# Performance work log

Measured on AMD Instinct MI355X. Metric: run time of the kernel, lower is better.

## Reference

```python
import jax, jax.numpy as jnp
import numpy as np

ALPHA = 0.2  # LeakyReLU negative slope
EPS = 1e-8


def setup_inputs() -> dict:
    key = jax.random.key(0)
    ks = jax.random.split(key, 7)
    N, Fin, Fout, E = 100000, 256, 128, 800000
    node_embedding = jax.random.normal(ks[0], (N, Fin), dtype=jnp.float32)
    adj_pos = jax.random.randint(ks[1], (2, E), 0, N, dtype=jnp.int64)
    adj_neg = jax.random.randint(ks[2], (2, E), 0, N, dtype=jnp.int64)
    edge_embedding = jax.random.normal(ks[3], (2, Fout), dtype=jnp.float32)
    Wr = jax.random.normal(ks[4], (2, Fin, Fout), dtype=jnp.float32) * 0.05
    a = jax.random.normal(ks[5], (1, 2 * Fout), dtype=jnp.float32) * 0.05
    bias = jax.random.normal(ks[6], (1, Fout), dtype=jnp.float32) * 0.05
    return dict(node_embedding=node_embedding, edge_embedding=edge_embedding,
                Wr=Wr, a=a, bias=bias, adj_pos=adj_pos, adj_neg=adj_neg)


def reference(node_embedding, edge_embedding, Wr, a, bias, adj_pos, adj_neg):
    N = node_embedding.shape[0]
    Fout = Wr.shape[2]
    # h_r = X @ Wr[r], then column-scale by edge_embedding[r] (== mm with diag)
    h_pos = (node_embedding @ Wr[0]) * edge_embedding[0]  # [N, Fout]
    h_neg = (node_embedding @ Wr[1]) * edge_embedding[1]  # [N, Fout]
    a_src = a[0, :Fout]  # attention weights for source half of concat
    a_dst = a[0, Fout:]  # attention weights for dest half

    def edge_scores(h, adj):
        # a . [h[src], h[dst]] computed as node-level dots then scalar gather
        s = h @ a_src  # [N]
        d = h @ a_dst  # [N]
        z = s[adj[0]] + d[adj[1]]  # [E]
        z = jnp.where(z > 0, z, ALPHA * z)  # LeakyReLU
        return jax.nn.sigmoid(z)

    e_pos = edge_scores(h_pos, adj_pos)  # [E_pos]
    e_neg = edge_scores(h_neg, adj_neg)  # [E_neg]

    # row-sum normalizer: spmm(edge, edge_e, ones) == segment_sum over row idx
    rows = jnp.concatenate([adj_pos[0], adj_neg[0]])
    e_all = jnp.concatenate([e_pos, e_neg])
    row_sum = jax.ops.segment_sum(e_all, rows, num_segments=N) + EPS  # [N]

    # weighted aggregation: out[i] = sum_{(i,j)} e_ij * h[j]
    agg = (jax.ops.segment_sum(e_pos[:, None] * h_pos[adj_pos[1]], adj_pos[0], num_segments=N)
           + jax.ops.segment_sum(e_neg[:, None] * h_neg[adj_neg[1]], adj_neg[0], num_segments=N))
    return agg / row_sum[:, None] + bias
```

## Files before the change

### kernel.cpp

```cpp
#include <hip/hip_runtime.h>

#define ALPHA 0.2f
#define EPSV 1e-8f
#define BUCK_BITS 8
#define BUCK (1 << BUCK_BITS)
#define CAP 5120
#define EPB_A 4096
#define EPT_A (EPB_A / 256)

typedef float f32x4 __attribute__((ext_vector_type(4)));
typedef short bf16x8 __attribute__((ext_vector_type(8)));

static __device__ __forceinline__ unsigned short f2bf(float f) {
    union { float f; unsigned int u; } c; c.f = f;
    unsigned int u = c.u;
    unsigned int round = ((u >> 16) & 1) + 0x7FFF;
    return (unsigned short)((u + round) >> 16);
}
static __device__ __forceinline__ float bflo(unsigned int u) {
    union { unsigned int u; float f; } c; c.u = u << 16; return c.f;
}
static __device__ __forceinline__ float bfhi(unsigned int u) {
    union { unsigned int u; float f; } c; c.u = u & 0xFFFF0000u; return c.f;
}

__global__ __launch_bounds__(256) void convB_binA_kernel(
    const float* __restrict__ Wr, uint4* __restrict__ Bp,
    const int* __restrict__ adj_pos, const int* __restrict__ adj_neg,
    int* __restrict__ bucketCount, unsigned int* __restrict__ edges_tmp,
    int N, int E)
{
    __shared__ int hist[512];
    __shared__ int base[512];
    __shared__ int cur[512];
    const int tid = threadIdx.x;

    if ((int)blockIdx.x < 32) {
        const int t = blockIdx.x * 256 + tid;
        const int kb  = t >> 8;
        const int col = t & 255;
        const int rel = col >> 7;
        const int cc  = col & 127;
        unsigned short v[8];
        #pragma unroll
        for (int jj = 0; jj < 8; ++jj) {
            const int k = kb * 8 + jj;
            v[jj] = f2bf(Wr[(size_t)rel * 256 * 128 + (size_t)k * 128 + cc]);
        }
        Bp[t] = *reinterpret_cast<const uint4*>(v);
        return;
    }

    const int bb = blockIdx.x - 32;
    const long long e0 = (long long)bb * EPB_A;
    const long long twoE = 2LL * E;

    hist[tid] = 0;
    hist[tid + 256] = 0;

    int esrc[EPT_A];
    unsigned int erec[EPT_A];
    #pragma unroll
    for (int k = 0; k < EPT_A; ++k) {
        const long long idx = e0 + (long long)k * 256 + tid;
        if (idx < twoE) {
            const int rel = (idx >= E) ? 1 : 0;
            const long long eidx = rel ? idx - E : idx;
            const int* __restrict__ adj = rel ? adj_neg : adj_pos;
            const int src = adj[eidx];
            const int dst = adj[E + eidx];
            esrc[k] = src;
            erec[k] = (unsigned int)dst | ((unsigned int)rel << 17) |
                      ((unsigned int)(src & (BUCK - 1)) << 18);
        } else {
            esrc[k] = -1;
        }
    }
    __syncthreads();

    #pragma unroll
    for (int k = 0; k < EPT_A; ++k)
        if (esrc[k] >= 0) atomicAdd(&hist[esrc[k] >> BUCK_BITS], 1);
    __syncthreads();

    {
        const int rot = (bb * 61) & 511;
        #pragma unroll
        for (int q = 0; q < 2; ++q) {
            const int t2 = (tid + q * 256 + rot) & 511;
            const int hv = hist[t2];
            base[t2] = hv ? atomicAdd(&bucketCount[t2], hv) : 0;
            cur[t2] = 0;
        }
    }
    __syncthreads();

    #pragma unroll
    for (int k = 0; k < EPT_A; ++k) {
        if (esrc[k] >= 0) {
            const int b = esrc[k] >> BUCK_BITS;
            const int r = atomicAdd(&cur[b], 1);
            const int pos = base[b] + r;
            if (pos < CAP)
                edges_tmp[(size_t)b * CAP + pos] = erec[k];
        }
    }
}

__global__ __launch_bounds__(128) void mfma_gemm_kernel(
    const float* __restrict__ X, const uint4* __restrict__ Bp,
    const float* __restrict__ ee, const float* __restrict__ a,
    unsigned int* __restrict__ h32, float* __restrict__ sd, int N)
{
    __shared__ unsigned short Alds[16 * 256];
    const int tid  = threadIdx.x;
    const int lane = tid & 63;
    const int wn   = tid >> 6;
    const int cl   = lane & 15;
    const int g    = lane >> 4;
    const int tile0 = blockIdx.x * 16;

    {
        float4 fa[4], fb[4];
        #pragma unroll
        for (int pass = 0; pass < 4; ++pass) {
            const int L  = pass * 128 + tid;
            const int r  = L >> 5;
            const int c8 = L & 31;
            const int row = tile0 + r;
            fa[pass] = make_float4(0.f, 0.f, 0.f, 0.f);
            fb[pass] = make_float4(0.f, 0.f, 0.f, 0.f);
            if (row < N) {
                const float* xp = &X[(size_t)row * 256 + c8 * 8];
                fa[pass] = *reinterpret_cast<const float4*>(xp);
                fb[pass] = *reinterpret_cast<const float4*>(xp + 4);
            }
        }
        #pragma unroll
        for (int pass = 0; pass < 4; ++pass) {
            const int L  = pass * 128 + tid;
            const int r  = L >> 5;
            const int c8 = L & 31;
            unsigned short v[8];
            v[0]=f2bf(fa[pass].x); v[1]=f2bf(fa[pass].y);
            v[2]=f2bf(fa[pass].z); v[3]=f2bf(fa[pass].w);
            v[4]=f2bf(fb[pass].x); v[5]=f2bf(fb[pass].y);
            v[6]=f2bf(fb[pass].z); v[7]=f2bf(fb[pass].w);
            const int su = c8 ^ (r & 7);
            *reinterpret_cast<bf16x8*>(&Alds[r * 256 + su * 8]) =
                *reinterpret_cast<const bf16x8*>(v);
        }
    }
    __syncthreads();

    f32x4 acc[8];
    #pragma unroll
    for (int ct = 0; ct < 8; ++ct)
        acc[ct] = (f32x4){0.f, 0.f, 0.f, 0.f};

    const int rl = cl;
    #pragma unroll
    for (int kc = 0; kc < 8; ++kc) {
        const int ku = kc * 4 + g;
        const bf16x8 af = *reinterpret_cast<const bf16x8*>(
            &Alds[rl * 256 + (ku ^ (rl & 7)) * 8]);
        bf16x8 bfr[8];
        #pragma unroll
        for (int ct = 0; ct < 8; ++ct) {
            const int col = wn * 128 + ct * 16 + cl;
            bfr[ct] = *reinterpret_cast<const bf16x8*>(Bp + ku * 256 + col);
        }
        #pragma unroll
        for (int ct = 0; ct < 8; ++ct)
            acc[ct] = __builtin_amdgcn_mfma_f32_16x16x32_bf16(
                af, bfr[ct], acc[ct], 0, 0, 0);
    }

    float eev[8], asv[8], adv[8];
    #pragma unroll
    for (int ct = 0; ct < 8; ++ct) {
        const int col = wn * 128 + ct * 16 + cl;
        const int cc  = col & 127;
        eev[ct] = ee[col];
        asv[ct] = a[cc];
        adv[ct] = a[128 + cc];
    }

    float s_acc[4], d_acc[4];
    #pragma unroll
    for (int reg = 0; reg < 4; ++reg) {
        const int row = tile0 + g * 4 + reg;
        const bool ok = row < N;
        float sp = 0.f, dp = 0.f;
        float vv[8];
        #pragma unroll
        for (int ct = 0; ct < 8; ++ct) {
            vv[ct] = acc[ct][reg] * eev[ct];
            sp += vv[ct] * asv[ct];
            dp += vv[ct] * adv[ct];
        }
        if (ok) {
            #pragma unroll
            for (int q = 0; q < 4; ++q) {
                const unsigned int u =
                    (unsigned int)f2bf(vv[2 * q]) |
                    ((unsigned int)f2bf(vv[2 * q + 1]) << 16);
                h32[((size_t)wn * N + row) * 64 + q * 16 + cl] = u;
            }
        }
        s_acc[reg] = sp;
        d_acc[reg] = dp;
    }
    #pragma unroll
    for (int reg = 0; reg < 4; ++reg) {
        float sp = s_acc[reg], dp = d_acc[reg];
        #pragma unroll
        for (int off = 1; off < 16; off <<= 1) {
            sp += __shfl_xor(sp, off);
            dp += __shfl_xor(dp, off);
        }
        if (cl == 0) {
            const int row = tile0 + g * 4 + reg;
            if (row < N) {
                sd[(size_t)wn * 2 * N + row]     = sp;
                sd[(size_t)wn * 2 * N + N + row] = dp;
            }
        }
    }
}

__global__ __launch_bounds__(512) void sortB_kernel(
    const int* __restrict__ bucketCount, const unsigned int* __restrict__ edges_tmp,
    const float* __restrict__ sd,
    uint2* __restrict__ edges_final,
    int* __restrict__ rowBeg, int* __restrict__ rowEnd,
    float* __restrict__ rowSum, int N)
{
    __shared__ int hist[BUCK];
    __shared__ int cur[BUCK];
    __shared__ int ssum[BUCK];
    __shared__ float sSrc[2][BUCK];
    __shared__ float rsLds[BUCK];
    const int tid = threadIdx.x;
    const int b   = blockIdx.x;
    const int s0  = b << BUCK_BITS;
    const size_t tb = (size_t)b * CAP;
    const int cnt = min(bucketCount[b], CAP);

    if (tid < BUCK) {
        hist[tid] = 0;
        rsLds[tid] = 0.f;
        const int gsrc = s0 + tid;
        sSrc[0][tid] = (gsrc < N) ? sd[gsrc] : 0.f;
        sSrc[1][tid] = (gsrc < N) ? sd[2 * (size_t)N + gsrc] : 0.f;
    }
    __syncthreads();
    for (int j = tid; j < cnt; j += 512)
        atomicAdd(&hist[edges_tmp[tb + j] >> 18], 1);
    __syncthreads();

    int h0 = 0, incl = 0;
    if (tid < BUCK) { h0 = hist[tid]; ssum[tid] = h0; incl = h0; }
    __syncthreads();
    for (int off = 1; off < BUCK; off <<= 1) {
        const int u = (tid < BUCK && tid >= off) ? ssum[tid - off] : 0;
        __syncthreads();
        if (tid < BUCK) { incl += u; ssum[tid] = incl; }
        __syncthreads();
    }
    if (tid < BUCK) {
        const int excl = incl - h0;
        cur[tid] = excl;
        const int gidx = s0 + tid;
        if (gidx < N) {
            rowBeg[gidx] = (int)tb + excl;
            rowEnd[gidx] = (int)tb + incl;
        }
    }
    __syncthreads();
    for (int j = tid; j < cnt; j += 512) {
        const unsigned int r = edges_tmp[tb + j];
        const int sl  = r >> 18;
        const int rel = (r >> 17) & 1;
        const int dst = r & 0x1FFFF;
        float z = sSrc[rel][sl] + sd[(size_t)rel * 2 * N + N + dst];
        z = z > 0.f ? z : ALPHA * z;
        const float ev = 1.f / (1.f + __expf(-z));
        const int pos = atomicAdd(&cur[sl], 1);
        atomicAdd(&rsLds[sl], ev);
        edges_final[tb + pos] =
            make_uint2((unsigned int)(rel * N + dst), __float_as_uint(ev));
    }
    __syncthreads();
    if (tid < BUCK) {
        const int gidx = s0 + tid;
        if (gidx < N) rowSum[gidx] = rsLds[tid];
    }
}

__global__ __launch_bounds__(256) void gather_kernel(
    const int* __restrict__ rowBeg, const int* __restrict__ rowEnd,
    const float* __restrict__ rowSum,
    const uint2* __restrict__ edges,
    const unsigned int* __restrict__ h32,
    const float* __restrict__ bias, float* __restrict__ out, int N)
{
    const long long gw = ((long long)blockIdx.x * blockDim.x + threadIdx.x) >> 6;
    const int lane = threadIdx.x & 63;
    if (gw >= N) return;
    const int n = (int)gw;

    const int beg = rowBeg[n];
    const int end = rowEnd[n];
    const unsigned loff = (unsigned)(lane << 2);
    const char* __restrict__ hb = (const char*)h32;

    float ax = 0.f, ay = 0.f;
    int j = beg;
    for (; j + 8 <= end; j += 8) {
        uint2 r[8];
        #pragma unroll
        for (int k = 0; k < 8; ++k) r[k] = edges[j + k];
        unsigned int hv[8];
        #pragma unroll
        for (int k = 0; k < 8; ++k)
            hv[k] = *reinterpret_cast<const unsigned int*>(
                hb + ((r[k].x << 8) + loff));
        #pragma unroll
        for (int k = 0; k < 8; ++k) {
            const float e = __uint_as_float(r[k].y);
            ax += e * bflo(hv[k]);
            ay += e * bfhi(hv[k]);
        }
    }
    for (; j + 4 <= end; j += 4) {
        uint2 r[4];
        #pragma unroll
        for (int k = 0; k < 4; ++k) r[k] = edges[j + k];
        unsigned int hv[4];
        #pragma unroll
        for (int k = 0; k < 4; ++k)
            hv[k] = *reinterpret_cast<const unsigned int*>(
                hb + ((r[k].x << 8) + loff));
        #pragma unroll
        for (int k = 0; k < 4; ++k) {
            const float e = __uint_as_float(r[k].y);
            ax += e * bflo(hv[k]);
            ay += e * bfhi(hv[k]);
        }
    }
    for (; j < end; ++j) {
        const uint2 r = edges[j];
        const unsigned int hv = *reinterpret_cast<const unsigned int*>(
            hb + ((r.x << 8) + loff));
        const float e = __uint_as_float(r.y);
        ax += e * bflo(hv);
        ay += e * bfhi(hv);
    }
    const float inv = 1.f / (rowSum[n] + EPSV);
    const int q  = lane >> 4;
    const int cl = lane & 15;
    const int c0 = q * 32 + cl;
    const int c1 = c0 + 16;
    out[(size_t)n * 128 + c0] = ax * inv + bias[c0];
    out[(size_t)n * 128 + c1] = ay * inv + bias[c1];
}

extern "C" void kernel_launch(void* const* d_in, const int* in_sizes, int n_in,
                              void* d_out, int out_size, void* d_ws, size_t ws_size,
                              hipStream_t stream) {
    const float* X      = (const float*)d_in[0];
    const float* ee     = (const float*)d_in[1];
    const float* Wr     = (const float*)d_in[2];
    const float* a      = (const float*)d_in[3];
    const float* bias   = (const float*)d_in[4];
    const int* adj_pos  = (const int*)d_in[5];
    const int* adj_neg  = (const int*)d_in[6];

    const int N = in_sizes[0] / 256;
    const int E = in_sizes[5] / 2;
    const int twoE = 2 * E;
    float* out = (float*)d_out;

    const int gemmBlocks = (N + 15) / 16;
    const int NBUCK = (N + BUCK - 1) >> BUCK_BITS;
    const int binBlocks = (twoE + EPB_A - 1) / EPB_A;

    char* ws = (char*)d_ws;
    uint4* Bp = (uint4*)ws;
    char* p = ws + 32 * 256 * 16;
    unsigned int* h32 = (unsigned int*)p; p += (size_t)2 * N * 64 * 4;
    float* sd         = (float*)p;  p += (size_t)4 * N * 4;
    int* bucketCount  = (int*)p;    p += 512 * 4;
    int* rowBeg       = (int*)p;    p += (size_t)N * 4;
    int* rowEnd       = (int*)p;    p += (size_t)N * 4;
    float* rowSum     = (float*)p;  p += (size_t)N * 4;
    p = (char*)(((uintptr_t)p + 15) & ~(uintptr_t)15);
    unsigned int* edges_tmp = (unsigned int*)p; p += (size_t)NBUCK * CAP * 4;
    uint2* edges_final = (uint2*)p; p += (size_t)NBUCK * CAP * 8;

    (void)hipMemsetAsync(bucketCount, 0, 512 * sizeof(int), stream);

    convB_binA_kernel<<<32 + binBlocks, 256, 0, stream>>>(
        Wr, Bp, adj_pos, adj_neg, bucketCount, edges_tmp, N, E);

    mfma_gemm_kernel<<<gemmBlocks, 128, 0, stream>>>(X, Bp, ee, a, h32, sd, N);

    sortB_kernel<<<NBUCK, 512, 0, stream>>>(
        bucketCount, edges_tmp, sd, edges_final, rowBeg, rowEnd, rowSum, N);

    gather_kernel<<<(int)(((long long)N * 64 + 255) / 256), 256, 0, stream>>>(
        rowBeg, rowEnd, rowSum, edges_final, h32, bias, out, N);
}
```

Baseline: 171.9 us.

## Fuse edge binning into GEMM kernel and double GEMM row tile

Weight conversion moves into its own small kernel, and edge binning is merged into the MFMA GEMM launch. Both the binning blocks and the GEMM blocks now come from one grid, so the two independent phases can run at the same time on the GPU. The GEMM block grows from 128 to 256 threads and covers 32 rows instead of 16, with four waves split 2x2 over rows and columns. This cuts the number of GEMM blocks and removes one dependency boundary between launches. In exchange, both code paths share one 16 KB shared-memory buffer and one register budget, which may lower occupancy for the lighter binning path.

```diff
diff --git a/kernel.cpp b/kernel.cpp
--- a/kernel.cpp
+++ b/kernel.cpp
@@ -24,107 +24,111 @@
     union { unsigned int u; float f; } c; c.u = u & 0xFFFF0000u; return c.f;
 }
 
-__global__ __launch_bounds__(256) void convB_binA_kernel(
-    const float* __restrict__ Wr, uint4* __restrict__ Bp,
+__global__ __launch_bounds__(256) void convB_kernel(
+    const float* __restrict__ Wr, uint4* __restrict__ Bp)
+{
+    const int t = blockIdx.x * blockDim.x + threadIdx.x;
+    if (t >= 32 * 256) return;
+    const int kb  = t >> 8;
+    const int col = t & 255;
+    const int rel = col >> 7;
+    const int cc  = col & 127;
+    unsigned short v[8];
+    #pragma unroll
+    for (int jj = 0; jj < 8; ++jj) {
+        const int k = kb * 8 + jj;
+        v[jj] = f2bf(Wr[(size_t)rel * 256 * 128 + (size_t)k * 128 + cc]);
+    }
+    Bp[t] = *reinterpret_cast<const uint4*>(v);
+}
+
+__global__ __launch_bounds__(256) void gemm_binA_kernel(
+    const float* __restrict__ X, const uint4* __restrict__ Bp,
+    const float* __restrict__ ee, const float* __restrict__ a,
+    unsigned int* __restrict__ h32, float* __restrict__ sd,
     const int* __restrict__ adj_pos, const int* __restrict__ adj_neg,
     int* __restrict__ bucketCount, unsigned int* __restrict__ edges_tmp,
-    int N, int E)
+    int N, int E, int binBlocks)
 {
-    __shared__ int hist[512];
-    __shared__ int base[512];
-    __shared__ int cur[512];
+    __shared__ char smem[16384];
     const int tid = threadIdx.x;
 
-    if ((int)blockIdx.x < 32) {
-        const int t = blockIdx.x * 256 + tid;
-        const int kb  = t >> 8;
-        const int col = t & 255;
-        const int rel = col >> 7;
-        const int cc  = col & 127;
-        unsigned short v[8];
-        #pragma unroll
-        for (int jj = 0; jj < 8; ++jj) {
-            const int k = kb * 8 + jj;
-            v[jj] = f2bf(Wr[(size_t)rel * 256 * 128 + (size_t)k * 128 + cc]);
-        }
-        Bp[t] = *reinterpret_cast<const uint4*>(v);
+    if ((int)blockIdx.x < binBlocks) {
+        int* hist = (int*)smem;
+        int* base = hist + 512;
+        int* cur  = base + 512;
+        const int bb = blockIdx.x;
+        const long long e0 = (long long)bb * EPB_A;
+        const long long twoE = 2LL * E;
+
+        hist[tid] = 0;
+        hist[tid + 256] = 0;
+
+        int esrc[EPT_A];
+        unsigned int erec[EPT_A];
+        #pragma unroll
+        for (int k = 0; k < EPT_A; ++k) {
+            const long long idx = e0 + (long long)k * 256 + tid;
+            if (idx < twoE) {
+                const int rel = (idx >= E) ? 1 : 0;
+                const long long eidx = rel ? idx - E : idx;
+                const int* __restrict__ adj = rel ? adj_neg : adj_pos;
+                const int src = adj[eidx];
+                const int dst = adj[E + eidx];
+                esrc[k] = src;
+                erec[k] = (unsigned int)dst | ((unsigned int)rel << 17) |
+                          ((unsigned int)(src & (BUCK - 1)) << 18);
+            } else {
+                esrc[k] = -1;
+            }
+        }
+        __syncthreads();
+
+        #pragma unroll
+        for (int k = 0; k < EPT_A; ++k)
+            if (esrc[k] >= 0) atomicAdd(&hist[esrc[k] >> BUCK_BITS], 1);
+        __syncthreads();
+
+        {
+            const int rot = (bb * 61) & 511;
+            #pragma unroll
+            for (int q = 0; q < 2; ++q) {
+                const int t2 = (tid + q * 256 + rot) & 511;
+                const int hv = hist[t2];
+                base[t2] = hv ? atomicAdd(&bucketCount[t2], hv) : 0;
+                cur[t2] = 0;
+            }
+        }
+        __syncthreads();
+
+        #pragma unroll
+        for (int k = 0; k < EPT_A; ++k) {
+            if (esrc[k] >= 0) {
+                const int b = esrc[k] >> BUCK_BITS;
+                const int r = atomicAdd(&cur[b], 1);
+                const int pos = base[b] + r;
+                if (pos < CAP)
+                    edges_tmp[(size_t)b * CAP + pos] = erec[k];
+            }
+        }
         return;
     }
 
-    const int bb = blockIdx.x - 32;
-    const long long e0 = (long long)bb * EPB_A;
-    const long long twoE = 2LL * E;
-
-    hist[tid] = 0;
-    hist[tid + 256] = 0;
-
-    int esrc[EPT_A];
-    unsigned int erec[EPT_A];
-    #pragma unroll
-    for (int k = 0; k < EPT_A; ++k) {
-        const long long idx = e0 + (long long)k * 256 + tid;
-        if (idx < twoE) {
-            const int rel = (idx >= E) ? 1 : 0;
-            const long long eidx = rel ? idx - E : idx;
-            const int* __restrict__ adj = rel ? adj_neg : adj_pos;
-            const int src = adj[eidx];
-            const int dst = adj[E + eidx];
-            esrc[k] = src;
-            erec[k] = (unsigned int)dst | ((unsigned int)rel << 17) |
-                      ((unsigned int)(src & (BUCK - 1)) << 18);
-        } else {
-            esrc[k] = -1;
-        }
-    }
-    __syncthreads();
-
-    #pragma unroll
-    for (int k = 0; k < EPT_A; ++k)
-        if (esrc[k] >= 0) atomicAdd(&hist[esrc[k] >> BUCK_BITS], 1);
-    __syncthreads();
-
-    {
-        const int rot = (bb * 61) & 511;
-        #pragma unroll
-        for (int q = 0; q < 2; ++q) {
-            const int t2 = (tid + q * 256 + rot) & 511;
-            const int hv = hist[t2];
-            base[t2] = hv ? atomicAdd(&bucketCount[t2], hv) : 0;
-            cur[t2] = 0;
-        }
-    }
-    __syncthreads();
-
-    #pragma unroll
-    for (int k = 0; k < EPT_A; ++k) {
-        if (esrc[k] >= 0) {
-            const int b = esrc[k] >> BUCK_BITS;
-            const int r = atomicAdd(&cur[b], 1);
-            const int pos = base[b] + r;
-            if (pos < CAP)
-                edges_tmp[(size_t)b * CAP + pos] = erec[k];
-        }
-    }
-}
-
-__global__ __launch_bounds__(128) void mfma_gemm_kernel(
-    const float* __restrict__ X, const uint4* __restrict__ Bp,
-    const float* __restrict__ ee, const float* __restrict__ a,
-    unsigned int* __restrict__ h32, float* __restrict__ sd, int N)
-{
-    __shared__ unsigned short Alds[16 * 256];
-    const int tid  = threadIdx.x;
+    unsigned short* Alds = (unsigned short*)smem;
     const int lane = tid & 63;
-    const int wn   = tid >> 6;
+    const int w    = tid >> 6;
+    const int wm   = w >> 1;
+    const int wn   = w & 1;
     const int cl   = lane & 15;
     const int g    = lane >> 4;
-    const int tile0 = blockIdx.x * 16;
+    const int gb   = blockIdx.x - binBlocks;
+    const int tile0 = gb * 32;
 
     {
         float4 fa[4], fb[4];
         #pragma unroll
         for (int pass = 0; pass < 4; ++pass) {
-            const int L  = pass * 128 + tid;
+            const int L  = pass * 256 + tid;
             const int r  = L >> 5;
             const int c8 = L & 31;
             const int row = tile0 + r;
@@ -138,7 +142,7 @@
         }
         #pragma unroll
         for (int pass = 0; pass < 4; ++pass) {
-            const int L  = pass * 128 + tid;
+            const int L  = pass * 256 + tid;
             const int r  = L >> 5;
             const int c8 = L & 31;
             unsigned short v[8];
@@ -158,7 +162,7 @@
     for (int ct = 0; ct < 8; ++ct)
         acc[ct] = (f32x4){0.f, 0.f, 0.f, 0.f};
 
-    const int rl = cl;
+    const int rl = wm * 16 + cl;
     #pragma unroll
     for (int kc = 0; kc < 8; ++kc) {
         const int ku = kc * 4 + g;
@@ -176,6 +180,7 @@
                 af, bfr[ct], acc[ct], 0, 0, 0);
     }
 
+    const int rt = gb * 2 + wm;
     float eev[8], asv[8], adv[8];
     #pragma unroll
     for (int ct = 0; ct < 8; ++ct) {
@@ -189,7 +194,7 @@
     float s_acc[4], d_acc[4];
     #pragma unroll
     for (int reg = 0; reg < 4; ++reg) {
-        const int row = tile0 + g * 4 + reg;
+        const int row = rt * 16 + g * 4 + reg;
         const bool ok = row < N;
         float sp = 0.f, dp = 0.f;
         float vv[8];
@@ -220,7 +225,7 @@
             dp += __shfl_xor(dp, off);
         }
         if (cl == 0) {
-            const int row = tile0 + g * 4 + reg;
+            const int row = rt * 16 + g * 4 + reg;
             if (row < N) {
                 sd[(size_t)wn * 2 * N + row]     = sp;
                 sd[(size_t)wn * 2 * N + N + row] = dp;
@@ -382,7 +387,7 @@
     const int twoE = 2 * E;
     float* out = (float*)d_out;
 
-    const int gemmBlocks = (N + 15) / 16;
+    const int gemmBlocks = (N + 31) / 32;
     const int NBUCK = (N + BUCK - 1) >> BUCK_BITS;
     const int binBlocks = (twoE + EPB_A - 1) / EPB_A;
 
@@ -401,10 +406,11 @@
 
     (void)hipMemsetAsync(bucketCount, 0, 512 * sizeof(int), stream);
 
-    convB_binA_kernel<<<32 + binBlocks, 256, 0, stream>>>(
-        Wr, Bp, adj_pos, adj_neg, bucketCount, edges_tmp, N, E);
-
-    mfma_gemm_kernel<<<gemmBlocks, 128, 0, stream>>>(X, Bp, ee, a, h32, sd, N);
+    convB_kernel<<<32, 256, 0, stream>>>(Wr, Bp);
+
+    gemm_binA_kernel<<<binBlocks + gemmBlocks, 256, 0, stream>>>(
+        X, Bp, ee, a, h32, sd, adj_pos, adj_neg, bucketCount, edges_tmp,
+        N, E, binBlocks);
 
     sortB_kernel<<<NBUCK, 512, 0, stream>>>(
         bucketCount, edges_tmp, sd, edges_final, rowBeg, rowEnd, rowSum, N);
```

Result: faster. 161.4 us (-6.1%).
